# Optimization experiments

Hardware: AMD Instinct MI355X
Metric: run time of the kernel (lower is better)

## Reference

```python
import jax, jax.numpy as jnp
import numpy as np

N_NODES = 50000
N_EDGES = 800000
IN_FEATS = 256
HIDDEN = 256
NUM_CLASSES = 64


def setup_inputs() -> dict:
    key = jax.random.key(0)
    k1, k2, k3, k4 = jax.random.split(key, 4)
    features = jax.random.normal(k1, (N_NODES, IN_FEATS), dtype=jnp.float32)
    edge_index = jax.random.randint(k2, (2, N_EDGES), 0, N_NODES, dtype=jnp.int32)
    W1 = jax.random.normal(k3, (IN_FEATS, HIDDEN), dtype=jnp.float32) * (1.0 / np.sqrt(IN_FEATS))
    b1 = jnp.zeros((HIDDEN,), dtype=jnp.float32)
    W2 = jax.random.normal(k4, (HIDDEN, NUM_CLASSES), dtype=jnp.float32) * (1.0 / np.sqrt(HIDDEN))
    b2 = jnp.zeros((NUM_CLASSES,), dtype=jnp.float32)
    return {"features": features, "edge_index": edge_index, "W1": W1, "b1": b1, "W2": W2, "b2": b2}


def reference(features, edge_index, W1, b1, W2, b2):
    # Two-layer GCN: h = A_hat @ relu(A_hat @ X W1 + b1) W2 + b2
    # A_hat uses symmetric degree normalization 1/sqrt(d_src * d_dst)
    N = features.shape[0]
    src, dst = edge_index[0], edge_index[1]
    ones = jnp.ones((src.shape[0],), dtype=features.dtype)
    deg_out = jax.ops.segment_sum(ones, src, num_segments=N)  # out-degree per node
    deg_in = jax.ops.segment_sum(ones, dst, num_segments=N)   # in-degree per node
    inv_sqrt_out = jax.lax.rsqrt(jnp.maximum(deg_out, 1.0))
    inv_sqrt_in = jax.lax.rsqrt(jnp.maximum(deg_in, 1.0))
    edge_norm = (inv_sqrt_out[src] * inv_sqrt_in[dst])[:, None]  # [E,1]

    def gcn_layer(x, W, b):
        h = x @ W                      # transform first (reduces message width)
        msg = h[src] * edge_norm       # [E, out]
        agg = jax.ops.segment_sum(msg, dst, num_segments=N)
        return agg + b

    h = jax.nn.relu(gcn_layer(features, W1, b1))
    return gcn_layer(h, W2, b2)
```

## Files before the change

### kernel.cpp

```cpp
#include <hip/hip_runtime.h>

#define NN 50000
#define MPAD 50048
#define NE 800000
#define SCAN_BLOCKS 49

typedef short short8 __attribute__((ext_vector_type(8)));
typedef float f32x4 __attribute__((ext_vector_type(4)));

__device__ __forceinline__ unsigned short f2bf(float x) {
    unsigned u = __builtin_bit_cast(unsigned, x);
    u += 0x7FFFu + ((u >> 16) & 1u);
    return (unsigned short)(u >> 16);
}
__device__ __forceinline__ float bf2f(unsigned short h) {
    unsigned u = ((unsigned)h) << 16;
    return __builtin_bit_cast(float, u);
}
__device__ __forceinline__ void gld16(const void* g, void* l) {
    __builtin_amdgcn_global_load_lds(
        (const __attribute__((address_space(1))) unsigned int*)g,
        (__attribute__((address_space(3))) unsigned int*)l, 16, 0, 0);
}


__global__ __launch_bounds__(256) void count_kernel(const int* __restrict__ src,
    const int* __restrict__ dst, int* __restrict__ cnt_out, int* __restrict__ cnt_in, int E)
{
    int e = blockIdx.x * 256 + threadIdx.x;
    if (e < E) {
        atomicAdd(&cnt_out[src[e]], 1);
        atomicAdd(&cnt_in[dst[e]], 1);
    }
}

__global__ __launch_bounds__(256) void inv_kernel(const int* __restrict__ cnt_out,
    const int* __restrict__ cnt_in, float* __restrict__ inv_out, float* __restrict__ inv_in, int n)
{
    int i = blockIdx.x * 256 + threadIdx.x;
    if (i < n) {
        inv_out[i] = rsqrtf(fmaxf((float)cnt_out[i], 1.0f));
        inv_in[i]  = rsqrtf(fmaxf((float)cnt_in[i], 1.0f));
    }
}

__global__ __launch_bounds__(256) void scanA_kernel(const int* __restrict__ cnt,
    int* __restrict__ bsum)
{
    __shared__ int sm[256];
    int b = blockIdx.x, tid = threadIdx.x;
    int base = b * 1024 + tid * 4;
    int s = 0;
    #pragma unroll
    for (int i = 0; i < 4; ++i) {
        int idx = base + i;
        if (idx < NN) s += cnt[idx];
    }
    sm[tid] = s;
    __syncthreads();
    for (int off = 128; off > 0; off >>= 1) {
        if (tid < off) sm[tid] += sm[tid + off];
        __syncthreads();
    }
    if (tid == 0) bsum[b] = sm[0];
}

__global__ __launch_bounds__(64) void scanB_kernel(const int* __restrict__ bsum,
    int* __restrict__ bexcl)
{
    int tid = threadIdx.x;
    int orig = (tid < SCAN_BLOCKS) ? bsum[tid] : 0;
    int v = orig;
    #pragma unroll
    for (int off = 1; off < 64; off <<= 1) {
        int u = __shfl_up(v, off, 64);
        if (tid >= off) v += u;
    }
    if (tid < SCAN_BLOCKS) bexcl[tid] = v - orig;
}

__global__ __launch_bounds__(256) void scanC_kernel(const int* __restrict__ cnt,
    const int* __restrict__ bexcl, int* __restrict__ rs)
{
    __shared__ int wsum[4];
    int b = blockIdx.x, tid = threadIdx.x;
    int lane = tid & 63, wv = tid >> 6;
    int base = b * 1024 + tid * 4;
    int v[4]; int s = 0;
    #pragma unroll
    for (int i = 0; i < 4; ++i) {
        int idx = base + i;
        v[i] = (idx < NN) ? cnt[idx] : 0;
        s += v[i];
    }
    int inc = s;
    #pragma unroll
    for (int off = 1; off < 64; off <<= 1) {
        int u = __shfl_up(inc, off, 64);
        if (lane >= off) inc += u;
    }
    if (lane == 63) wsum[wv] = inc;
    __syncthreads();
    int wo = 0;
    for (int i = 0; i < wv; ++i) wo += wsum[i];
    int run = wo + (inc - s) + bexcl[b];
    #pragma unroll
    for (int i = 0; i < 4; ++i) {
        int idx = base + i;
        if (idx < NN) { rs[idx] = run; run += v[i]; }
    }
}

__global__ __launch_bounds__(256) void fill_kernel(const int* __restrict__ src,
    const int* __restrict__ dst, int* __restrict__ rs, int* __restrict__ csr_src, int E)
{
    int e = blockIdx.x * 256 + threadIdx.x;
    if (e < E) {
        int slot = atomicAdd(&rs[dst[e]], 1);
        csr_src[slot] = src[e];
    }
}

__global__ __launch_bounds__(256) void splitX_kernel(const float* __restrict__ X,
    unsigned short* __restrict__ Xh, unsigned short* __restrict__ Xl)
{
    int i = blockIdx.x * 256 + threadIdx.x;
    if (i >= NN * 32) return;
    int r = i >> 5, c = i & 31;
    const float* src = X + (size_t)r * 256 + c * 8;
    float4 a0 = *(const float4*)src;
    float4 a1 = *(const float4*)(src + 4);
    float xs[8] = {a0.x, a0.y, a0.z, a0.w, a1.x, a1.y, a1.z, a1.w};
    short8 hv, lv;
    #pragma unroll
    for (int t = 0; t < 8; ++t) {
        unsigned short h = f2bf(xs[t]);
        hv[t] = (short)h;
        lv[t] = (short)f2bf(xs[t] - bf2f(h));
    }
    size_t off = (size_t)r * 256 + (c >> 3) * 64 + (((c & 7) ^ (r & 7)) * 8);
    *(short8*)&Xh[off] = hv;
    *(short8*)&Xl[off] = lv;
}

__global__ __launch_bounds__(256) void splitW_kernel(const float* __restrict__ W,
    unsigned short* __restrict__ BT, int N)
{
    int i = blockIdx.x * 256 + threadIdx.x;
    if (i >= N * 32) return;
    int col = i >> 5, kc = i & 31;
    short8 hv, lv;
    #pragma unroll
    for (int j = 0; j < 8; ++j) {
        float x = W[(size_t)(kc * 8 + j) * N + col];
        unsigned short h = f2bf(x);
        hv[j] = (short)h;
        lv[j] = (short)f2bf(x - bf2f(h));
    }
    size_t base = (size_t)col * 512;
    size_t o = (kc >> 3) * 64 + (((kc & 7) ^ (col & 7)) * 8);
    *(short8*)&BT[base + o] = hv;
    *(short8*)&BT[base + 256 + o] = lv;
}

template<int BN, bool SWZ_OUT>
__global__ __launch_bounds__(256) void gemm_sp_kernel(
    const unsigned short* __restrict__ Ah, const unsigned short* __restrict__ Al,
    const unsigned short* __restrict__ BT, const float* __restrict__ inv_out,
    unsigned short* __restrict__ C, int M, int Ntot)
{
    constexpr int WN = BN / 2;
    constexpr int NF = WN / 16;
    constexpr int BI = BN / 32;
    __shared__ unsigned short Ash[128 * 64];
    __shared__ unsigned short Asl[128 * 64];
    __shared__ unsigned short Bsh[BN * 64];
    __shared__ unsigned short Bsl[BN * 64];
    const int tid = threadIdx.x;
    const int w = tid >> 6, lane = tid & 63;
    const int wm = w >> 1, wn = w & 1;
    const int r = lane & 15, kg = lane >> 4;
    const int rowbase = blockIdx.x * 128;
    const int colbase = blockIdx.y * BN;

    f32x4 acc[4][NF] = {};

    for (int kb = 0; kb < 4; ++kb) {
        #pragma unroll
        for (int i = 0; i < 4; ++i) {
            int ct = (w * 4 + i) * 64 + lane;
            int row = ct >> 3, c = ct & 7;
            size_t goff = (size_t)(rowbase + row) * 256 + kb * 64 + c * 8;
            gld16(Ah + goff, (unsigned short*)Ash + (size_t)ct * 8);
            gld16(Al + goff, (unsigned short*)Asl + (size_t)ct * 8);
        }
        #pragma unroll
        for (int i = 0; i < BI; ++i) {
            int ct = (w * BI + i) * 64 + lane;
            int col = ct >> 3, c = ct & 7;
            size_t goff = (size_t)(colbase + col) * 512 + kb * 64 + c * 8;
            gld16(BT + goff, (unsigned short*)Bsh + (size_t)ct * 8);
            gld16(BT + goff + 256, (unsigned short*)Bsl + (size_t)ct * 8);
        }
        __syncthreads();
        #pragma unroll
        for (int ks = 0; ks < 2; ++ks) {
            short8 ahf[4], alf[4];
            #pragma unroll
            for (int mf = 0; mf < 4; ++mf) {
                int row = wm * 64 + mf * 16 + r;
                int lo = row * 64 + (((ks * 4 + kg) ^ (row & 7)) * 8);
                ahf[mf] = *(const short8*)&Ash[lo];
                alf[mf] = *(const short8*)&Asl[lo];
            }
            #pragma unroll
            for (int nf = 0; nf < NF; ++nf) {
                int col = wn * WN + nf * 16 + r;
                int lo = col * 64 + (((ks * 4 + kg) ^ (col & 7)) * 8);
                short8 bh = *(const short8*)&Bsh[lo];
                short8 bl = *(const short8*)&Bsl[lo];
                #pragma unroll
                for (int mf = 0; mf < 4; ++mf) {
                    acc[mf][nf] = __builtin_amdgcn_mfma_f32_16x16x32_bf16(ahf[mf], bh, acc[mf][nf], 0, 0, 0);
                    acc[mf][nf] = __builtin_amdgcn_mfma_f32_16x16x32_bf16(alf[mf], bh, acc[mf][nf], 0, 0, 0);
                    acc[mf][nf] = __builtin_amdgcn_mfma_f32_16x16x32_bf16(ahf[mf], bl, acc[mf][nf], 0, 0, 0);
                }
            }
        }
        __syncthreads();
    }

    #pragma unroll
    for (int mf = 0; mf < 4; ++mf) {
        #pragma unroll
        for (int reg = 0; reg < 4; ++reg) {
            int orow = rowbase + wm * 64 + mf * 16 + kg * 4 + reg;
            if (orow >= M) continue;
            float sc = inv_out[orow];
            #pragma unroll
            for (int nf = 0; nf < NF; ++nf) {
                int ocol = colbase + wn * WN + nf * 16 + r;
                unsigned short v = f2bf(acc[mf][nf][reg] * sc);
                if (SWZ_OUT) {
                    size_t idx = (size_t)orow * 256 + (ocol >> 6) * 64
                               + ((((ocol >> 3) & 7) ^ (orow & 7)) * 8) + (ocol & 7);
                    C[idx] = v;
                } else {
                    C[(size_t)orow * Ntot + ocol] = v;
                }
            }
        }
    }
}

__global__ __launch_bounds__(256) void gather256_kernel(const unsigned short* __restrict__ t1s,
    const int* __restrict__ csr_src, const int* __restrict__ rs,
    const float* __restrict__ inv_in, const float* __restrict__ b1,
    unsigned short* __restrict__ Ah2, unsigned short* __restrict__ Al2)
{
    int n = (int)((blockIdx.x * 256 + threadIdx.x) >> 6);
    int lane = threadIdx.x & 63;
    if (n >= NN) return;
    int begin = (n == 0) ? 0 : rs[n - 1];
    int end = rs[n];
    int c = lane >> 1, h = lane & 1;
    int cc = c & 7;
    int sub = (c >> 3) * 64 + h * 4;
    float a0 = 0.f, a1 = 0.f, a2 = 0.f, a3 = 0.f;
    int j = begin;
    for (; j + 4 <= end; j += 4) {
        int s0 = csr_src[j], s1 = csr_src[j + 1], s2 = csr_src[j + 2], s3 = csr_src[j + 3];
        ushort4 v0 = *(const ushort4*)&t1s[(size_t)s0 * 256 + sub + ((cc ^ (s0 & 7)) * 8)];
        ushort4 v1 = *(const ushort4*)&t1s[(size_t)s1 * 256 + sub + ((cc ^ (s1 & 7)) * 8)];
        ushort4 v2 = *(const ushort4*)&t1s[(size_t)s2 * 256 + sub + ((cc ^ (s2 & 7)) * 8)];
        ushort4 v3 = *(const ushort4*)&t1s[(size_t)s3 * 256 + sub + ((cc ^ (s3 & 7)) * 8)];
        a0 += bf2f(v0.x); a1 += bf2f(v0.y); a2 += bf2f(v0.z); a3 += bf2f(v0.w);
        a0 += bf2f(v1.x); a1 += bf2f(v1.y); a2 += bf2f(v1.z); a3 += bf2f(v1.w);
        a0 += bf2f(v2.x); a1 += bf2f(v2.y); a2 += bf2f(v2.z); a3 += bf2f(v2.w);
        a0 += bf2f(v3.x); a1 += bf2f(v3.y); a2 += bf2f(v3.z); a3 += bf2f(v3.w);
    }
    for (; j < end; ++j) {
        int s = csr_src[j];
        ushort4 v = *(const ushort4*)&t1s[(size_t)s * 256 + sub + ((cc ^ (s & 7)) * 8)];
        a0 += bf2f(v.x); a1 += bf2f(v.y); a2 += bf2f(v.z); a3 += bf2f(v.w);
    }
    float win = inv_in[n];
    int k0 = c * 8 + h * 4;
    float4 bb = *(const float4*)&b1[k0];
    float x0 = fmaxf(fmaf(a0, win, bb.x), 0.f);
    float x1 = fmaxf(fmaf(a1, win, bb.y), 0.f);
    float x2 = fmaxf(fmaf(a2, win, bb.z), 0.f);
    float x3 = fmaxf(fmaf(a3, win, bb.w), 0.f);
    unsigned short h0 = f2bf(x0), h1 = f2bf(x1), h2 = f2bf(x2), h3 = f2bf(x3);
    ushort4 hv = {h0, h1, h2, h3};
    ushort4 lv = {f2bf(x0 - bf2f(h0)), f2bf(x1 - bf2f(h1)),
                  f2bf(x2 - bf2f(h2)), f2bf(x3 - bf2f(h3))};
    size_t off = (size_t)n * 256 + sub + ((cc ^ (n & 7)) * 8);
    *(ushort4*)&Ah2[off] = hv;
    *(ushort4*)&Al2[off] = lv;
}

__global__ __launch_bounds__(256) void gather64_kernel(const unsigned short* __restrict__ t2,
    const int* __restrict__ csr_src, const int* __restrict__ rs,
    const float* __restrict__ inv_in, const float* __restrict__ b2,
    float* __restrict__ out)
{
    int n = (int)((blockIdx.x * 256 + threadIdx.x) >> 6);
    int lane = threadIdx.x & 63;
    if (n >= NN) return;
    int begin = (n == 0) ? 0 : rs[n - 1];
    int end = rs[n];
    float acc = 0.f;
    int j = begin;
    for (; j + 4 <= end; j += 4) {
        int s0 = csr_src[j], s1 = csr_src[j + 1], s2 = csr_src[j + 2], s3 = csr_src[j + 3];
        float v0 = bf2f(t2[(size_t)s0 * 64 + lane]);
        float v1 = bf2f(t2[(size_t)s1 * 64 + lane]);
        float v2 = bf2f(t2[(size_t)s2 * 64 + lane]);
        float v3 = bf2f(t2[(size_t)s3 * 64 + lane]);
        acc += v0; acc += v1; acc += v2; acc += v3;
    }
    for (; j < end; ++j) {
        int s = csr_src[j];
        acc += bf2f(t2[(size_t)s * 64 + lane]);
    }
    out[(size_t)n * 64 + lane] = fmaf(acc, inv_in[n], b2[lane]);
}

extern "C" void kernel_launch(void* const* d_in, const int* in_sizes, int n_in,
                              void* d_out, int out_size, void* d_ws, size_t ws_size,
                              hipStream_t stream)
{
    const float* features = (const float*)d_in[0];
    const int*   edge_index = (const int*)d_in[1];
    const float* W1 = (const float*)d_in[2];
    const float* b1 = (const float*)d_in[3];
    const float* W2 = (const float*)d_in[4];
    const float* b2 = (const float*)d_in[5];
    float* out = (float*)d_out;
    const int* src = edge_index;
    const int* dst = edge_index + NE;

    char* p = (char*)d_ws;
    int* cnt_out = (int*)p;            p += (size_t)NN * 4;
    int* cnt_in  = (int*)p;            p += (size_t)NN * 4;
    float* inv_out = (float*)p;        p += (size_t)NN * 4;
    float* inv_in  = (float*)p;        p += (size_t)NN * 4;
    int* rs      = (int*)p;            p += (size_t)NN * 4;
    int* csr_src = (int*)p;            p += (size_t)NE * 4;
    int* bsum    = (int*)p;            p += 64 * 4;
    int* bexcl   = (int*)p;            p += 64 * 4;
    unsigned short* W1T = (unsigned short*)p;  p += (size_t)256 * 512 * 2;
    unsigned short* W2T = (unsigned short*)p;  p += (size_t)64 * 512 * 2;
    unsigned short* Xh  = (unsigned short*)p;  p += (size_t)MPAD * 256 * 2;
    unsigned short* Xl  = (unsigned short*)p;  p += (size_t)MPAD * 256 * 2;
    unsigned short* t1s = (unsigned short*)p;  p += (size_t)NN * 256 * 2;
    unsigned short* Ah2 = (unsigned short*)p;  p += (size_t)MPAD * 256 * 2;
    unsigned short* Al2 = (unsigned short*)p;  p += (size_t)MPAD * 256 * 2;
    unsigned short* t2  = (unsigned short*)p;  p += (size_t)NN * 64 * 2;

    hipMemsetAsync(cnt_out, 0, 2 * (size_t)NN * sizeof(int), stream);

    count_kernel<<<(NE + 255) / 256, 256, 0, stream>>>(src, dst, cnt_out, cnt_in, NE);
    inv_kernel<<<(NN + 255) / 256, 256, 0, stream>>>(cnt_out, cnt_in, inv_out, inv_in, NN);
    scanA_kernel<<<SCAN_BLOCKS, 256, 0, stream>>>(cnt_in, bsum);
    scanB_kernel<<<1, 64, 0, stream>>>(bsum, bexcl);
    scanC_kernel<<<SCAN_BLOCKS, 256, 0, stream>>>(cnt_in, bexcl, rs);
    fill_kernel<<<(NE + 255) / 256, 256, 0, stream>>>(src, dst, rs, csr_src, NE);

    splitX_kernel<<<(NN * 32 + 255) / 256, 256, 0, stream>>>(features, Xh, Xl);
    splitW_kernel<<<(256 * 32 + 255) / 256, 256, 0, stream>>>(W1, W1T, 256);
    splitW_kernel<<<(64 * 32 + 255) / 256, 256, 0, stream>>>(W2, W2T, 64);

    gemm_sp_kernel<128, true><<<dim3(MPAD / 128, 2), 256, 0, stream>>>(
        Xh, Xl, W1T, inv_out, t1s, NN, 256);

    gather256_kernel<<<(NN * 64 + 255) / 256, 256, 0, stream>>>(
        t1s, csr_src, rs, inv_in, b1, Ah2, Al2);

    gemm_sp_kernel<64, false><<<dim3(MPAD / 128, 1), 256, 0, stream>>>(
        Ah2, Al2, W2T, inv_out, t2, NN, 64);

    gather64_kernel<<<(NN * 64 + 255) / 256, 256, 0, stream>>>(
        t2, csr_src, rs, inv_in, b2, out);
}
```

Measured before the change: 320.6 us.

## Split gather kernels into feature chunks with edge-parallel lanes and shuffle reduction

The aggregation kernels are restructured so that each block handles one 64-byte feature chunk (8 chunks for the 256-wide layer, 2 for the 64-wide layer). Within a wave, four lane groups process four edges at once and combine their results with cross-lane shuffles. The first GEMM now writes a plain row-major output instead of a swizzled one. The intent is to shrink the per-node working set of each pass so L2 reuse improves, and to expose more edge-level parallelism. The cost is 8x more blocks, index lists read once per chunk, and only a quarter of the lanes doing the final stores.

```diff
diff --git a/kernel.cpp b/kernel.cpp
--- a/kernel.cpp
+++ b/kernel.cpp
@@ -163,7 +163,7 @@
     *(short8*)&BT[base + 256 + o] = lv;
 }
 
-template<int BN, bool SWZ_OUT>
+template<int BN>
 __global__ __launch_bounds__(256) void gemm_sp_kernel(
     const unsigned short* __restrict__ Ah, const unsigned short* __restrict__ Al,
     const unsigned short* __restrict__ BT, const float* __restrict__ inv_out,
@@ -240,91 +240,97 @@
             #pragma unroll
             for (int nf = 0; nf < NF; ++nf) {
                 int ocol = colbase + wn * WN + nf * 16 + r;
-                unsigned short v = f2bf(acc[mf][nf][reg] * sc);
-                if (SWZ_OUT) {
-                    size_t idx = (size_t)orow * 256 + (ocol >> 6) * 64
-                               + ((((ocol >> 3) & 7) ^ (orow & 7)) * 8) + (ocol & 7);
-                    C[idx] = v;
-                } else {
-                    C[(size_t)orow * Ntot + ocol] = v;
-                }
+                C[(size_t)orow * Ntot + ocol] = f2bf(acc[mf][nf][reg] * sc);
             }
         }
     }
 }
 
-__global__ __launch_bounds__(256) void gather256_kernel(const unsigned short* __restrict__ t1s,
+__global__ __launch_bounds__(256) void gather256c_kernel(const unsigned short* __restrict__ t1,
     const int* __restrict__ csr_src, const int* __restrict__ rs,
     const float* __restrict__ inv_in, const float* __restrict__ b1,
     unsigned short* __restrict__ Ah2, unsigned short* __restrict__ Al2)
 {
-    int n = (int)((blockIdx.x * 256 + threadIdx.x) >> 6);
+    int bid = blockIdx.x;
+    int chunk = bid & 7;
+    int n = (bid >> 3) * 4 + (threadIdx.x >> 6);
+    if (n >= NN) return;
     int lane = threadIdx.x & 63;
-    if (n >= NN) return;
+    int g = lane >> 4;
+    int fl = lane & 15;
     int begin = (n == 0) ? 0 : rs[n - 1];
     int end = rs[n];
-    int c = lane >> 1, h = lane & 1;
-    int cc = c & 7;
-    int sub = (c >> 3) * 64 + h * 4;
-    float a0 = 0.f, a1 = 0.f, a2 = 0.f, a3 = 0.f;
+    const unsigned short* base = t1 + chunk * 32 + fl * 2;
+    float a0 = 0.f, a1 = 0.f;
     int j = begin;
     for (; j + 4 <= end; j += 4) {
-        int s0 = csr_src[j], s1 = csr_src[j + 1], s2 = csr_src[j + 2], s3 = csr_src[j + 3];
-        ushort4 v0 = *(const ushort4*)&t1s[(size_t)s0 * 256 + sub + ((cc ^ (s0 & 7)) * 8)];
-        ushort4 v1 = *(const ushort4*)&t1s[(size_t)s1 * 256 + sub + ((cc ^ (s1 & 7)) * 8)];
-        ushort4 v2 = *(const ushort4*)&t1s[(size_t)s2 * 256 + sub + ((cc ^ (s2 & 7)) * 8)];
-        ushort4 v3 = *(const ushort4*)&t1s[(size_t)s3 * 256 + sub + ((cc ^ (s3 & 7)) * 8)];
-        a0 += bf2f(v0.x); a1 += bf2f(v0.y); a2 += bf2f(v0.z); a3 += bf2f(v0.w);
-        a0 += bf2f(v1.x); a1 += bf2f(v1.y); a2 += bf2f(v1.z); a3 += bf2f(v1.w);
-        a0 += bf2f(v2.x); a1 += bf2f(v2.y); a2 += bf2f(v2.z); a3 += bf2f(v2.w);
-        a0 += bf2f(v3.x); a1 += bf2f(v3.y); a2 += bf2f(v3.z); a3 += bf2f(v3.w);
-    }
-    for (; j < end; ++j) {
-        int s = csr_src[j];
-        ushort4 v = *(const ushort4*)&t1s[(size_t)s * 256 + sub + ((cc ^ (s & 7)) * 8)];
-        a0 += bf2f(v.x); a1 += bf2f(v.y); a2 += bf2f(v.z); a3 += bf2f(v.w);
-    }
-    float win = inv_in[n];
-    int k0 = c * 8 + h * 4;
-    float4 bb = *(const float4*)&b1[k0];
-    float x0 = fmaxf(fmaf(a0, win, bb.x), 0.f);
-    float x1 = fmaxf(fmaf(a1, win, bb.y), 0.f);
-    float x2 = fmaxf(fmaf(a2, win, bb.z), 0.f);
-    float x3 = fmaxf(fmaf(a3, win, bb.w), 0.f);
-    unsigned short h0 = f2bf(x0), h1 = f2bf(x1), h2 = f2bf(x2), h3 = f2bf(x3);
-    ushort4 hv = {h0, h1, h2, h3};
-    ushort4 lv = {f2bf(x0 - bf2f(h0)), f2bf(x1 - bf2f(h1)),
-                  f2bf(x2 - bf2f(h2)), f2bf(x3 - bf2f(h3))};
-    size_t off = (size_t)n * 256 + sub + ((cc ^ (n & 7)) * 8);
-    *(ushort4*)&Ah2[off] = hv;
-    *(ushort4*)&Al2[off] = lv;
-}
-
-__global__ __launch_bounds__(256) void gather64_kernel(const unsigned short* __restrict__ t2,
+        int s = csr_src[j + g];
+        unsigned v = *(const unsigned*)&base[(size_t)s * 256];
+        a0 += bf2f((unsigned short)(v & 0xffffu));
+        a1 += bf2f((unsigned short)(v >> 16));
+    }
+    if (j + g < end) {
+        int s = csr_src[j + g];
+        unsigned v = *(const unsigned*)&base[(size_t)s * 256];
+        a0 += bf2f((unsigned short)(v & 0xffffu));
+        a1 += bf2f((unsigned short)(v >> 16));
+    }
+    a0 += __shfl_xor(a0, 16); a1 += __shfl_xor(a1, 16);
+    a0 += __shfl_xor(a0, 32); a1 += __shfl_xor(a1, 32);
+    if (g == 0) {
+        float win = inv_in[n];
+        int f0 = chunk * 32 + fl * 2;
+        float2 bb = *(const float2*)&b1[f0];
+        float x0 = fmaxf(fmaf(a0, win, bb.x), 0.f);
+        float x1 = fmaxf(fmaf(a1, win, bb.y), 0.f);
+        unsigned short h0 = f2bf(x0), h1 = f2bf(x1);
+        ushort2 hv = {h0, h1};
+        ushort2 lv = {f2bf(x0 - bf2f(h0)), f2bf(x1 - bf2f(h1))};
+        int kb = f0 >> 6, pp = f0 & 63, c = pp >> 3, e = pp & 7;
+        size_t off = (size_t)n * 256 + kb * 64 + ((c ^ (n & 7)) * 8) + e;
+        *(ushort2*)&Ah2[off] = hv;
+        *(ushort2*)&Al2[off] = lv;
+    }
+}
+
+__global__ __launch_bounds__(256) void gather64c_kernel(const unsigned short* __restrict__ t2,
     const int* __restrict__ csr_src, const int* __restrict__ rs,
     const float* __restrict__ inv_in, const float* __restrict__ b2,
     float* __restrict__ out)
 {
-    int n = (int)((blockIdx.x * 256 + threadIdx.x) >> 6);
+    int bid = blockIdx.x;
+    int chunk = bid & 1;
+    int n = (bid >> 1) * 4 + (threadIdx.x >> 6);
+    if (n >= NN) return;
     int lane = threadIdx.x & 63;
-    if (n >= NN) return;
+    int g = lane >> 4;
+    int fl = lane & 15;
     int begin = (n == 0) ? 0 : rs[n - 1];
     int end = rs[n];
-    float acc = 0.f;
+    const unsigned short* base = t2 + chunk * 32 + fl * 2;
+    float a0 = 0.f, a1 = 0.f;
     int j = begin;
     for (; j + 4 <= end; j += 4) {
-        int s0 = csr_src[j], s1 = csr_src[j + 1], s2 = csr_src[j + 2], s3 = csr_src[j + 3];
-        float v0 = bf2f(t2[(size_t)s0 * 64 + lane]);
-        float v1 = bf2f(t2[(size_t)s1 * 64 + lane]);
-        float v2 = bf2f(t2[(size_t)s2 * 64 + lane]);
-        float v3 = bf2f(t2[(size_t)s3 * 64 + lane]);
-        acc += v0; acc += v1; acc += v2; acc += v3;
-    }
-    for (; j < end; ++j) {
-        int s = csr_src[j];
-        acc += bf2f(t2[(size_t)s * 64 + lane]);
-    }
-    out[(size_t)n * 64 + lane] = fmaf(acc, inv_in[n], b2[lane]);
+        int s = csr_src[j + g];
+        unsigned v = *(const unsigned*)&base[(size_t)s * 64];
+        a0 += bf2f((unsigned short)(v & 0xffffu));
+        a1 += bf2f((unsigned short)(v >> 16));
+    }
+    if (j + g < end) {
+        int s = csr_src[j + g];
+        unsigned v = *(const unsigned*)&base[(size_t)s * 64];
+        a0 += bf2f((unsigned short)(v & 0xffffu));
+        a1 += bf2f((unsigned short)(v >> 16));
+    }
+    a0 += __shfl_xor(a0, 16); a1 += __shfl_xor(a1, 16);
+    a0 += __shfl_xor(a0, 32); a1 += __shfl_xor(a1, 32);
+    if (g == 0) {
+        float win = inv_in[n];
+        int f0 = chunk * 32 + fl * 2;
+        float2 bb = *(const float2*)&b2[f0];
+        float2 o = {fmaf(a0, win, bb.x), fmaf(a1, win, bb.y)};
+        *(float2*)&out[(size_t)n * 64 + f0] = o;
+    }
 }
 
 extern "C" void kernel_launch(void* const* d_in, const int* in_sizes, int n_in,
@@ -354,7 +360,7 @@
     unsigned short* W2T = (unsigned short*)p;  p += (size_t)64 * 512 * 2;
     unsigned short* Xh  = (unsigned short*)p;  p += (size_t)MPAD * 256 * 2;
     unsigned short* Xl  = (unsigned short*)p;  p += (size_t)MPAD * 256 * 2;
-    unsigned short* t1s = (unsigned short*)p;  p += (size_t)NN * 256 * 2;
+    unsigned short* t1  = (unsigned short*)p;  p += (size_t)NN * 256 * 2;
     unsigned short* Ah2 = (unsigned short*)p;  p += (size_t)MPAD * 256 * 2;
     unsigned short* Al2 = (unsigned short*)p;  p += (size_t)MPAD * 256 * 2;
     unsigned short* t2  = (unsigned short*)p;  p += (size_t)NN * 64 * 2;
@@ -372,15 +378,15 @@
     splitW_kernel<<<(256 * 32 + 255) / 256, 256, 0, stream>>>(W1, W1T, 256);
     splitW_kernel<<<(64 * 32 + 255) / 256, 256, 0, stream>>>(W2, W2T, 64);
 
-    gemm_sp_kernel<128, true><<<dim3(MPAD / 128, 2), 256, 0, stream>>>(
-        Xh, Xl, W1T, inv_out, t1s, NN, 256);
-
-    gather256_kernel<<<(NN * 64 + 255) / 256, 256, 0, stream>>>(
-        t1s, csr_src, rs, inv_in, b1, Ah2, Al2);
-
-    gemm_sp_kernel<64, false><<<dim3(MPAD / 128, 1), 256, 0, stream>>>(
+    gemm_sp_kernel<128><<<dim3(MPAD / 128, 2), 256, 0, stream>>>(
+        Xh, Xl, W1T, inv_out, t1, NN, 256);
+
+    gather256c_kernel<<<((NN + 3) / 4) * 8, 256, 0, stream>>>(
+        t1, csr_src, rs, inv_in, b1, Ah2, Al2);
+
+    gemm_sp_kernel<64><<<dim3(MPAD / 128, 1), 256, 0, stream>>>(
         Ah2, Al2, W2T, inv_out, t2, NN, 64);
 
-    gather64_kernel<<<(NN * 64 + 255) / 256, 256, 0, stream>>>(
+    gather64c_kernel<<<((NN + 3) / 4) * 2, 256, 0, stream>>>(
         t2, csr_src, rs, inv_in, b2, out);
 }
```

Result: slower. 473.7 us (+47.8%).

## Store t1 row-major, unroll gathers by eight, use nontemporal stores

Applied to the files above, without the earlier changes.

The first GEMM now writes t1 in plain row-major layout instead of the swizzled layout. gather256 then reads contiguous 8-byte chunks per lane, and it applies the swizzle only when writing Ah2 and Al2. Both gather kernels unroll the edge loop from 4 to 8 to keep more loads in flight. Their outputs use nontemporal stores to avoid polluting the cache. The GEMM epilogue's scattered 2-byte stores are unchanged apart from losing the swizzle arithmetic, and the higher unroll may raise register pressure.

```diff
diff --git a/kernel.cpp b/kernel.cpp
--- a/kernel.cpp
+++ b/kernel.cpp
@@ -21,6 +21,10 @@
     __builtin_amdgcn_global_load_lds(
         (const __attribute__((address_space(1))) unsigned int*)g,
         (__attribute__((address_space(3))) unsigned int*)l, 16, 0, 0);
+}
+__device__ __forceinline__ void nt_store8(void* p, ushort4 v) {
+    __builtin_nontemporal_store(__builtin_bit_cast(unsigned long long, v),
+                                (unsigned long long*)p);
 }
 
 
@@ -163,7 +167,7 @@
     *(short8*)&BT[base + 256 + o] = lv;
 }
 
-template<int BN, bool SWZ_OUT>
+template<int BN>
 __global__ __launch_bounds__(256) void gemm_sp_kernel(
     const unsigned short* __restrict__ Ah, const unsigned short* __restrict__ Al,
     const unsigned short* __restrict__ BT, const float* __restrict__ inv_out,
@@ -240,20 +244,13 @@
             #pragma unroll
             for (int nf = 0; nf < NF; ++nf) {
                 int ocol = colbase + wn * WN + nf * 16 + r;
-                unsigned short v = f2bf(acc[mf][nf][reg] * sc);
-                if (SWZ_OUT) {
-                    size_t idx = (size_t)orow * 256 + (ocol >> 6) * 64
-                               + ((((ocol >> 3) & 7) ^ (orow & 7)) * 8) + (ocol & 7);
-                    C[idx] = v;
-                } else {
-                    C[(size_t)orow * Ntot + ocol] = v;
-                }
+                C[(size_t)orow * Ntot + ocol] = f2bf(acc[mf][nf][reg] * sc);
             }
         }
     }
 }
 
-__global__ __launch_bounds__(256) void gather256_kernel(const unsigned short* __restrict__ t1s,
+__global__ __launch_bounds__(256) void gather256_kernel(const unsigned short* __restrict__ t1,
     const int* __restrict__ csr_src, const int* __restrict__ rs,
     const float* __restrict__ inv_in, const float* __restrict__ b1,
     unsigned short* __restrict__ Ah2, unsigned short* __restrict__ Al2)
@@ -263,30 +260,36 @@
     if (n >= NN) return;
     int begin = (n == 0) ? 0 : rs[n - 1];
     int end = rs[n];
-    int c = lane >> 1, h = lane & 1;
-    int cc = c & 7;
-    int sub = (c >> 3) * 64 + h * 4;
     float a0 = 0.f, a1 = 0.f, a2 = 0.f, a3 = 0.f;
     int j = begin;
-    for (; j + 4 <= end; j += 4) {
-        int s0 = csr_src[j], s1 = csr_src[j + 1], s2 = csr_src[j + 2], s3 = csr_src[j + 3];
-        ushort4 v0 = *(const ushort4*)&t1s[(size_t)s0 * 256 + sub + ((cc ^ (s0 & 7)) * 8)];
-        ushort4 v1 = *(const ushort4*)&t1s[(size_t)s1 * 256 + sub + ((cc ^ (s1 & 7)) * 8)];
-        ushort4 v2 = *(const ushort4*)&t1s[(size_t)s2 * 256 + sub + ((cc ^ (s2 & 7)) * 8)];
-        ushort4 v3 = *(const ushort4*)&t1s[(size_t)s3 * 256 + sub + ((cc ^ (s3 & 7)) * 8)];
+    for (; j + 8 <= end; j += 8) {
+        int s0 = csr_src[j],     s1 = csr_src[j + 1], s2 = csr_src[j + 2], s3 = csr_src[j + 3];
+        int s4 = csr_src[j + 4], s5 = csr_src[j + 5], s6 = csr_src[j + 6], s7 = csr_src[j + 7];
+        ushort4 v0 = *(const ushort4*)&t1[(size_t)s0 * 256 + lane * 4];
+        ushort4 v1 = *(const ushort4*)&t1[(size_t)s1 * 256 + lane * 4];
+        ushort4 v2 = *(const ushort4*)&t1[(size_t)s2 * 256 + lane * 4];
+        ushort4 v3 = *(const ushort4*)&t1[(size_t)s3 * 256 + lane * 4];
+        ushort4 v4 = *(const ushort4*)&t1[(size_t)s4 * 256 + lane * 4];
+        ushort4 v5 = *(const ushort4*)&t1[(size_t)s5 * 256 + lane * 4];
+        ushort4 v6 = *(const ushort4*)&t1[(size_t)s6 * 256 + lane * 4];
+        ushort4 v7 = *(const ushort4*)&t1[(size_t)s7 * 256 + lane * 4];
         a0 += bf2f(v0.x); a1 += bf2f(v0.y); a2 += bf2f(v0.z); a3 += bf2f(v0.w);
         a0 += bf2f(v1.x); a1 += bf2f(v1.y); a2 += bf2f(v1.z); a3 += bf2f(v1.w);
         a0 += bf2f(v2.x); a1 += bf2f(v2.y); a2 += bf2f(v2.z); a3 += bf2f(v2.w);
         a0 += bf2f(v3.x); a1 += bf2f(v3.y); a2 += bf2f(v3.z); a3 += bf2f(v3.w);
+        a0 += bf2f(v4.x); a1 += bf2f(v4.y); a2 += bf2f(v4.z); a3 += bf2f(v4.w);
+        a0 += bf2f(v5.x); a1 += bf2f(v5.y); a2 += bf2f(v5.z); a3 += bf2f(v5.w);
+        a0 += bf2f(v6.x); a1 += bf2f(v6.y); a2 += bf2f(v6.z); a3 += bf2f(v6.w);
+        a0 += bf2f(v7.x); a1 += bf2f(v7.y); a2 += bf2f(v7.z); a3 += bf2f(v7.w);
     }
     for (; j < end; ++j) {
         int s = csr_src[j];
-        ushort4 v = *(const ushort4*)&t1s[(size_t)s * 256 + sub + ((cc ^ (s & 7)) * 8)];
+        ushort4 v = *(const ushort4*)&t1[(size_t)s * 256 + lane * 4];
         a0 += bf2f(v.x); a1 += bf2f(v.y); a2 += bf2f(v.z); a3 += bf2f(v.w);
     }
     float win = inv_in[n];
-    int k0 = c * 8 + h * 4;
-    float4 bb = *(const float4*)&b1[k0];
+    int f0 = lane * 4;
+    float4 bb = *(const float4*)&b1[f0];
     float x0 = fmaxf(fmaf(a0, win, bb.x), 0.f);
     float x1 = fmaxf(fmaf(a1, win, bb.y), 0.f);
     float x2 = fmaxf(fmaf(a2, win, bb.z), 0.f);
@@ -295,9 +298,10 @@
     ushort4 hv = {h0, h1, h2, h3};
     ushort4 lv = {f2bf(x0 - bf2f(h0)), f2bf(x1 - bf2f(h1)),
                   f2bf(x2 - bf2f(h2)), f2bf(x3 - bf2f(h3))};
-    size_t off = (size_t)n * 256 + sub + ((cc ^ (n & 7)) * 8);
-    *(ushort4*)&Ah2[off] = hv;
-    *(ushort4*)&Al2[off] = lv;
+    int kb = f0 >> 6, c = (f0 >> 3) & 7, e = f0 & 7;
+    size_t off = (size_t)n * 256 + kb * 64 + ((c ^ (n & 7)) * 8) + e;
+    nt_store8(&Ah2[off], hv);
+    nt_store8(&Al2[off], lv);
 }
 
 __global__ __launch_bounds__(256) void gather64_kernel(const unsigned short* __restrict__ t2,
@@ -312,19 +316,26 @@
     int end = rs[n];
     float acc = 0.f;
     int j = begin;
-    for (; j + 4 <= end; j += 4) {
-        int s0 = csr_src[j], s1 = csr_src[j + 1], s2 = csr_src[j + 2], s3 = csr_src[j + 3];
+    for (; j + 8 <= end; j += 8) {
+        int s0 = csr_src[j],     s1 = csr_src[j + 1], s2 = csr_src[j + 2], s3 = csr_src[j + 3];
+        int s4 = csr_src[j + 4], s5 = csr_src[j + 5], s6 = csr_src[j + 6], s7 = csr_src[j + 7];
         float v0 = bf2f(t2[(size_t)s0 * 64 + lane]);
         float v1 = bf2f(t2[(size_t)s1 * 64 + lane]);
         float v2 = bf2f(t2[(size_t)s2 * 64 + lane]);
         float v3 = bf2f(t2[(size_t)s3 * 64 + lane]);
+        float v4 = bf2f(t2[(size_t)s4 * 64 + lane]);
+        float v5 = bf2f(t2[(size_t)s5 * 64 + lane]);
+        float v6 = bf2f(t2[(size_t)s6 * 64 + lane]);
+        float v7 = bf2f(t2[(size_t)s7 * 64 + lane]);
         acc += v0; acc += v1; acc += v2; acc += v3;
+        acc += v4; acc += v5; acc += v6; acc += v7;
     }
     for (; j < end; ++j) {
         int s = csr_src[j];
         acc += bf2f(t2[(size_t)s * 64 + lane]);
     }
-    out[(size_t)n * 64 + lane] = fmaf(acc, inv_in[n], b2[lane]);
+    float o = fmaf(acc, inv_in[n], b2[lane]);
+    __builtin_nontemporal_store(o, &out[(size_t)n * 64 + lane]);
 }
 
 extern "C" void kernel_launch(void* const* d_in, const int* in_sizes, int n_in,
@@ -354,7 +365,7 @@
     unsigned short* W2T = (unsigned short*)p;  p += (size_t)64 * 512 * 2;
     unsigned short* Xh  = (unsigned short*)p;  p += (size_t)MPAD * 256 * 2;
     unsigned short* Xl  = (unsigned short*)p;  p += (size_t)MPAD * 256 * 2;
-    unsigned short* t1s = (unsigned short*)p;  p += (size_t)NN * 256 * 2;
+    unsigned short* t1  = (unsigned short*)p;  p += (size_t)NN * 256 * 2;
     unsigned short* Ah2 = (unsigned short*)p;  p += (size_t)MPAD * 256 * 2;
     unsigned short* Al2 = (unsigned short*)p;  p += (size_t)MPAD * 256 * 2;
     unsigned short* t2  = (unsigned short*)p;  p += (size_t)NN * 64 * 2;
@@ -372,13 +383,13 @@
     splitW_kernel<<<(256 * 32 + 255) / 256, 256, 0, stream>>>(W1, W1T, 256);
     splitW_kernel<<<(64 * 32 + 255) / 256, 256, 0, stream>>>(W2, W2T, 64);
 
-    gemm_sp_kernel<128, true><<<dim3(MPAD / 128, 2), 256, 0, stream>>>(
-        Xh, Xl, W1T, inv_out, t1s, NN, 256);
+    gemm_sp_kernel<128><<<dim3(MPAD / 128, 2), 256, 0, stream>>>(
+        Xh, Xl, W1T, inv_out, t1, NN, 256);
 
     gather256_kernel<<<(NN * 64 + 255) / 256, 256, 0, stream>>>(
-        t1s, csr_src, rs, inv_in, b1, Ah2, Al2);
-
-    gemm_sp_kernel<64, false><<<dim3(MPAD / 128, 1), 256, 0, stream>>>(
+        t1, csr_src, rs, inv_in, b1, Ah2, Al2);
+
+    gemm_sp_kernel<64><<<dim3(MPAD / 128, 1), 256, 0, stream>>>(
         Ah2, Al2, W2T, inv_out, t2, NN, 64);
 
     gather64_kernel<<<(NN * 64 + 255) / 256, 256, 0, stream>>>(
```

Measured after the change: 326.9 us. About the same (+2.0%).
